# Optimization experiments

Hardware: AMD Instinct MI355X
Metric: run time of the kernel (lower is better)

Reference implementation:

```python
import jax, jax.numpy as jnp
import numpy as np

B = 4          # per_gpu_batch_size
P = 16         # n_contexts
N = B * P      # fused passage dim = 64
L = 512        # seq_len
H = 768        # hidden_size
S = 16         # sentence spans per passage


def setup_inputs() -> dict:
    key = jax.random.key(0)
    k1, k2, k3 = jax.random.split(key, 3)
    hidden_states = jax.random.normal(k1, (N, L, H), jnp.float32)
    # nn.Linear weight [out, in]; original init std=1.0 saturates tanh, use 0.02 scale for sane numerics
    dense_w = jax.random.normal(k2, (H, H), jnp.float32) * 0.02
    dense_b = jnp.zeros((H,), jnp.float32)
    attention_mask = jnp.ones((N, L), jnp.int32)
    # strictly increasing boundaries -> S non-empty, ragged, contiguous spans per passage
    r = jnp.sort(jax.random.randint(k3, (N, S + 1), 0, L - S), axis=-1) + jnp.arange(S + 1, dtype=jnp.int32)
    spans = jnp.stack([r[:, :-1], r[:, 1:]], axis=-1).astype(jnp.int32)  # [N, S, 2]
    return dict(hidden_states=hidden_states, dense_w=dense_w, dense_b=dense_b,
                attention_mask=attention_mask, spans=spans)


def reference(hidden_states, dense_w, dense_b, attention_mask, spans):
    # sentence_spans branch: token_tensor = hidden_states (all tokens)
    # pooled_output = activation(dense(token_tensor)); cls_norm_type == 'none' -> no norm
    pooled = jnp.tanh(jnp.einsum('nlh,oh->nlo', hidden_states, dense_w) + dense_b)  # [N, L, H]
    pooled_output_passages = pooled[:, 0]  # [N, H]
    # ragged per-span mean pooling, vectorized as a masked segment reduce
    pos = jnp.arange(L, dtype=jnp.int32)                         # [L]
    start = spans[..., 0][..., None]                             # [N, S, 1]
    end = spans[..., 1][..., None]                               # [N, S, 1]
    m = ((pos >= start) & (pos < end)).astype(pooled.dtype)      # [N, S, L]
    sums = jnp.einsum('nsl,nlh->nsh', m, pooled)                 # [N, S, H]
    counts = (spans[..., 1] - spans[..., 0]).astype(pooled.dtype)[..., None]  # [N, S, 1]
    sentence_embeddings = (sums / counts).reshape(N * S, H)      # [N*S, H]
    # all S spans valid per passage -> mask of zeros (0 = valid in original code)
    sentence_mask = jnp.zeros((N, S), jnp.float32)
    return pooled_output_passages, sentence_embeddings, sentence_mask
```

## Files before the change

### kernel.cpp

```cpp
#include <hip/hip_runtime.h>
#include <hip/hip_bf16.h>

#define NPASS 64
#define LSEQ  512
#define HDIM  768
#define NSPAN 16
#define MTOT  (NPASS*LSEQ)
#define OFF_SENT (NPASS*HDIM)
#define A_ELEMS (MTOT*HDIM)
#define W_ELEMS (HDIM*HDIM)

#define BM 128
#define BN 128
#define BK 32
#define NK (HDIM/BK)

typedef __bf16 bf16x8 __attribute__((ext_vector_type(8)));
typedef float  f32x4  __attribute__((ext_vector_type(4)));

__device__ inline unsigned short f2bf(float f) {
  __hip_bfloat16 h = __float2bfloat16(f);
  unsigned short u; __builtin_memcpy(&u, &h, 2); return u;
}

__device__ inline float fast_tanh(float x) {
  const float ax = fabsf(x);
  const float t  = __expf(-2.0f * ax);
  const float r  = (1.0f - t) * __builtin_amdgcn_rcpf(1.0f + t);
  return copysignf(r, x);
}

__global__ __launch_bounds__(256) void convert_kernel(
    const float* __restrict__ A, const float* __restrict__ W,
    unsigned short* __restrict__ Ab, unsigned short* __restrict__ Wb)
{
  const long long i = ((long long)blockIdx.x * 256 + threadIdx.x) * 8;
  const float* src; unsigned short* dst; long long off;
  if (i < A_ELEMS) { src = A; dst = Ab; off = i; }
  else             { src = W; dst = Wb; off = i - A_ELEMS; }
  const float4 a = *(const float4*)(src + off);
  const float4 b = *(const float4*)(src + off + 4);
  union { unsigned short us[8]; uint4 v; } o;
  o.us[0]=f2bf(a.x); o.us[1]=f2bf(a.y); o.us[2]=f2bf(a.z); o.us[3]=f2bf(a.w);
  o.us[4]=f2bf(b.x); o.us[5]=f2bf(b.y); o.us[6]=f2bf(b.z); o.us[7]=f2bf(b.w);
  *(uint4*)(dst + off) = o.v;
}

__global__ __launch_bounds__(256) void gemm_fused_kernel(
    const unsigned short* __restrict__ Ab,
    const unsigned short* __restrict__ Wb,
    const float* __restrict__ bias,
    const int* __restrict__ spans,
    float* __restrict__ out)
{
  __shared__ __align__(16) unsigned short As[2][BM*BK];
  __shared__ __align__(16) unsigned short Bs[2][BN*BK];
  __shared__ int   sp_st[NSPAN], sp_en[NSPAN];
  __shared__ float inv_s[NSPAN];
  __shared__ short sid_l[BM];
  __shared__ float bias_s[BN];

  const int tid  = threadIdx.x;
  const int wave = tid >> 6;
  const int lane = tid & 63;
  const int quad = lane >> 4;
  const int lr   = lane & 15;
  const int wm   = wave >> 1;
  const int wn   = wave & 1;
  const int tile_m = blockIdx.x * BM;
  const int tile_n = blockIdx.y * BN;
  const int npass  = tile_m >> 9;
  const int l0     = tile_m & 511;

  const int lrow = lane >> 2;
  const int lcol = (lane & 3) * 8;

  auto stage = [&](int k, int buf) {
    const int k0 = k * BK;
    #pragma unroll
    for (int j = 0; j < 4; ++j) {
      const int seg = wave * 4 + j;
      if (seg < 8) {
        const unsigned short* g =
            Ab + (size_t)(tile_m + seg * 16 + lrow) * HDIM + (k0 + lcol);
        __builtin_amdgcn_global_load_lds(
            (const __attribute__((address_space(1))) void*)g,
            (__attribute__((address_space(3))) void*)(As[buf] + seg * 512),
            16, 0, 0);
      } else {
        const int s2 = seg - 8;
        const unsigned short* g =
            Wb + (size_t)(tile_n + s2 * 16 + lrow) * HDIM + (k0 + lcol);
        __builtin_amdgcn_global_load_lds(
            (const __attribute__((address_space(1))) void*)g,
            (__attribute__((address_space(3))) void*)(Bs[buf] + s2 * 512),
            16, 0, 0);
      }
    }
  };

  stage(0, 0);
  if (tid < NSPAN) {
    const int st = spans[(npass * NSPAN + tid) * 2 + 0];
    const int en = spans[(npass * NSPAN + tid) * 2 + 1];
    sp_st[tid] = st; sp_en[tid] = en; inv_s[tid] = 1.0f / (float)(en - st);
  }
  if (tid >= 128 && tid < 128 + BN) bias_s[tid - 128] = bias[tile_n + tid - 128];
  __syncthreads();
  if (tid < BM) {
    const int l = l0 + tid;
    short s = -1;
    #pragma unroll
    for (int i = 0; i < NSPAN; ++i)
      if (l >= sp_st[i] && l < sp_en[i]) s = (short)i;
    sid_l[tid] = s;
  }

  f32x4 acc[4][4];
  #pragma unroll
  for (int i = 0; i < 4; ++i)
    #pragma unroll
    for (int j = 0; j < 4; ++j)
      acc[i][j] = (f32x4){0.f, 0.f, 0.f, 0.f};

  for (int k = 0; k < NK; ++k) {
    const int cur = k & 1;
    if (k + 1 < NK) stage(k + 1, cur ^ 1);

    bf16x8 af[4], bf[4];
    #pragma unroll
    for (int mt = 0; mt < 4; ++mt)
      af[mt] = *(const bf16x8*)(As[cur] + ((wm * 64 + mt * 16 + lr) * BK + quad * 8));
    #pragma unroll
    for (int nt = 0; nt < 4; ++nt)
      bf[nt] = *(const bf16x8*)(Bs[cur] + ((wn * 64 + nt * 16 + lr) * BK + quad * 8));

    #pragma unroll
    for (int mt = 0; mt < 4; ++mt)
      #pragma unroll
      for (int nt = 0; nt < 4; ++nt)
        acc[mt][nt] = __builtin_amdgcn_mfma_f32_16x16x32_bf16(
            af[mt], bf[nt], acc[mt][nt], 0, 0, 0);

    __syncthreads();
  }

  #pragma unroll
  for (int nt = 0; nt < 4; ++nt) {
    const int lcolo = wn * 64 + nt * 16 + lr;
    const int col   = tile_n + lcolo;
    const float bv  = bias_s[lcolo];
    float* sent_col = out + OFF_SENT + (size_t)(npass * NSPAN) * HDIM + col;
    #pragma unroll
    for (int mt = 0; mt < 4; ++mt) {
      const int rowbase = wm * 64 + mt * 16 + quad * 4;
      int prev = -1; float run = 0.f;
      #pragma unroll
      for (int r = 0; r < 4; ++r) {
        const int lrw = rowbase + r;
        const float v = fast_tanh(acc[mt][nt][r] + bv);
        if (l0 == 0 && lrw == 0) out[(size_t)npass * HDIM + col] = v;
        const int s = sid_l[lrw];
        if (s != prev) {
          if (prev >= 0) unsafeAtomicAdd(sent_col + (size_t)prev * HDIM, run * inv_s[prev]);
          prev = s; run = 0.f;
        }
        run += v;
      }
      if (prev >= 0) unsafeAtomicAdd(sent_col + (size_t)prev * HDIM, run * inv_s[prev]);
    }
  }
}

extern "C" void kernel_launch(void* const* d_in, const int* in_sizes, int n_in,
                              void* d_out, int out_size, void* d_ws, size_t ws_size,
                              hipStream_t stream) {
  const float* hs  = (const float*)d_in[0];
  const float* w   = (const float*)d_in[1];
  const float* bsc = (const float*)d_in[2];
  const int* spans = (const int*)d_in[4];
  float* out = (float*)d_out;

  unsigned short* Ab = (unsigned short*)d_ws;
  unsigned short* Wb = Ab + A_ELEMS;

  hipMemsetAsync(d_out, 0, (size_t)out_size * sizeof(float), stream);

  convert_kernel<<<dim3((A_ELEMS + W_ELEMS) / 8 / 256), dim3(256), 0, stream>>>(
      hs, w, Ab, Wb);

  dim3 grid(MTOT / BM, HDIM / BN);
  gemm_fused_kernel<<<grid, dim3(256), 0, stream>>>(Ab, Wb, bsc, spans, out);
}
```

Measured before the change: 268.0 us.

## Fuse fp32-to-bf16 activation conversion into GEMM staging with swizzled LDS

Removes the standalone pass that converted the full activation tensor to bf16. The GEMM now stages fp32 activations directly into LDS and converts them to bf16 in registers before the MFMA. XOR swizzles are added to the A and B LDS layouts to reduce bank conflicts. This saves a full read/write pass over the activations, but doubles the A bytes read per N-tile and doubles the LDS footprint for A, which may reduce occupancy.

```diff
diff --git a/kernel.cpp b/kernel.cpp
--- a/kernel.cpp
+++ b/kernel.cpp
@@ -7,7 +7,6 @@
 #define NSPAN 16
 #define MTOT  (NPASS*LSEQ)
 #define OFF_SENT (NPASS*HDIM)
-#define A_ELEMS (MTOT*HDIM)
 #define W_ELEMS (HDIM*HDIM)
 
 #define BM 128
@@ -16,6 +15,7 @@
 #define NK (HDIM/BK)
 
 typedef __bf16 bf16x8 __attribute__((ext_vector_type(8)));
+typedef __bf16 bf16x4 __attribute__((ext_vector_type(4)));
 typedef float  f32x4  __attribute__((ext_vector_type(4)));
 
 __device__ inline unsigned short f2bf(float f) {
@@ -30,30 +30,33 @@
   return copysignf(r, x);
 }
 
-__global__ __launch_bounds__(256) void convert_kernel(
-    const float* __restrict__ A, const float* __restrict__ W,
-    unsigned short* __restrict__ Ab, unsigned short* __restrict__ Wb)
+__device__ inline bf16x8 cvt8(f32x4 lo, f32x4 hi) {
+  union { bf16x4 h[2]; bf16x8 v; } u;
+  u.h[0] = __builtin_convertvector(lo, bf16x4);
+  u.h[1] = __builtin_convertvector(hi, bf16x4);
+  return u.v;
+}
+
+__global__ __launch_bounds__(256) void convert_w_kernel(
+    const float* __restrict__ W, unsigned short* __restrict__ Wb)
 {
-  const long long i = ((long long)blockIdx.x * 256 + threadIdx.x) * 8;
-  const float* src; unsigned short* dst; long long off;
-  if (i < A_ELEMS) { src = A; dst = Ab; off = i; }
-  else             { src = W; dst = Wb; off = i - A_ELEMS; }
-  const float4 a = *(const float4*)(src + off);
-  const float4 b = *(const float4*)(src + off + 4);
+  const int i = (blockIdx.x * 256 + threadIdx.x) * 8;
+  const float4 a = *(const float4*)(W + i);
+  const float4 b = *(const float4*)(W + i + 4);
   union { unsigned short us[8]; uint4 v; } o;
   o.us[0]=f2bf(a.x); o.us[1]=f2bf(a.y); o.us[2]=f2bf(a.z); o.us[3]=f2bf(a.w);
   o.us[4]=f2bf(b.x); o.us[5]=f2bf(b.y); o.us[6]=f2bf(b.z); o.us[7]=f2bf(b.w);
-  *(uint4*)(dst + off) = o.v;
+  *(uint4*)(Wb + i) = o.v;
 }
 
 __global__ __launch_bounds__(256) void gemm_fused_kernel(
-    const unsigned short* __restrict__ Ab,
+    const float* __restrict__ A,
     const unsigned short* __restrict__ Wb,
     const float* __restrict__ bias,
     const int* __restrict__ spans,
     float* __restrict__ out)
 {
-  __shared__ __align__(16) unsigned short As[2][BM*BK];
+  __shared__ __align__(16) float          As[2][BM*BK];
   __shared__ __align__(16) unsigned short Bs[2][BN*BK];
   __shared__ int   sp_st[NSPAN], sp_en[NSPAN];
   __shared__ float inv_s[NSPAN];
@@ -72,25 +75,25 @@
   const int npass  = tile_m >> 9;
   const int l0     = tile_m & 511;
 
-  const int lrow = lane >> 2;
-  const int lcol = (lane & 3) * 8;
-
   auto stage = [&](int k, int buf) {
     const int k0 = k * BK;
     #pragma unroll
-    for (int j = 0; j < 4; ++j) {
-      const int seg = wave * 4 + j;
-      if (seg < 8) {
-        const unsigned short* g =
-            Ab + (size_t)(tile_m + seg * 16 + lrow) * HDIM + (k0 + lcol);
+    for (int j = 0; j < 6; ++j) {
+      const int seg = j * 4 + wave;
+      if (seg < 16) {
+        const int row = seg * 8 + (lane >> 3);
+        const int gs  = (lane & 7) ^ ((lane >> 3) & 7);
+        const float* g = A + (size_t)(tile_m + row) * HDIM + (k0 + gs * 4);
         __builtin_amdgcn_global_load_lds(
             (const __attribute__((address_space(1))) void*)g,
-            (__attribute__((address_space(3))) void*)(As[buf] + seg * 512),
+            (__attribute__((address_space(3))) void*)(As[buf] + seg * 256),
             16, 0, 0);
       } else {
-        const int s2 = seg - 8;
+        const int s2  = seg - 16;
+        const int row = s2 * 16 + (lane >> 2);
+        const int gs  = (lane & 3) ^ ((lane >> 3) & 3);
         const unsigned short* g =
-            Wb + (size_t)(tile_n + s2 * 16 + lrow) * HDIM + (k0 + lcol);
+            Wb + (size_t)(tile_n + row) * HDIM + (k0 + gs * 8);
         __builtin_amdgcn_global_load_lds(
             (const __attribute__((address_space(1))) void*)g,
             (__attribute__((address_space(3))) void*)(Bs[buf] + s2 * 512),
@@ -127,20 +130,29 @@
     const int cur = k & 1;
     if (k + 1 < NK) stage(k + 1, cur ^ 1);
 
-    bf16x8 af[4], bf[4];
-    #pragma unroll
-    for (int mt = 0; mt < 4; ++mt)
-      af[mt] = *(const bf16x8*)(As[cur] + ((wm * 64 + mt * 16 + lr) * BK + quad * 8));
-    #pragma unroll
-    for (int nt = 0; nt < 4; ++nt)
-      bf[nt] = *(const bf16x8*)(Bs[cur] + ((wn * 64 + nt * 16 + lr) * BK + quad * 8));
+    bf16x8 af[4], bfr[4];
+    #pragma unroll
+    for (int mt = 0; mt < 4; ++mt) {
+      const int r  = wm * 64 + mt * 16 + lr;
+      const int sw = r & 7;
+      const float* base = As[cur] + r * BK;
+      const f32x4 lo = *(const f32x4*)(base + (((quad * 2    ) ^ sw) * 4));
+      const f32x4 hi = *(const f32x4*)(base + (((quad * 2 + 1) ^ sw) * 4));
+      af[mt] = cvt8(lo, hi);
+    }
+    #pragma unroll
+    for (int nt = 0; nt < 4; ++nt) {
+      const int r = wn * 64 + nt * 16 + lr;
+      const int g = quad ^ ((r >> 1) & 3);
+      bfr[nt] = *(const bf16x8*)(Bs[cur] + (r * BK + g * 8));
+    }
 
     #pragma unroll
     for (int mt = 0; mt < 4; ++mt)
       #pragma unroll
       for (int nt = 0; nt < 4; ++nt)
         acc[mt][nt] = __builtin_amdgcn_mfma_f32_16x16x32_bf16(
-            af[mt], bf[nt], acc[mt][nt], 0, 0, 0);
+            af[mt], bfr[nt], acc[mt][nt], 0, 0, 0);
 
     __syncthreads();
   }
@@ -181,14 +193,12 @@
   const int* spans = (const int*)d_in[4];
   float* out = (float*)d_out;
 
-  unsigned short* Ab = (unsigned short*)d_ws;
-  unsigned short* Wb = Ab + A_ELEMS;
+  unsigned short* Wb = (unsigned short*)d_ws;
 
   hipMemsetAsync(d_out, 0, (size_t)out_size * sizeof(float), stream);
 
-  convert_kernel<<<dim3((A_ELEMS + W_ELEMS) / 8 / 256), dim3(256), 0, stream>>>(
-      hs, w, Ab, Wb);
+  convert_w_kernel<<<dim3(W_ELEMS / 8 / 256), dim3(256), 0, stream>>>(w, Wb);
 
   dim3 grid(MTOT / BM, HDIM / BN);
-  gemm_fused_kernel<<<grid, dim3(256), 0, stream>>>(Ab, Wb, bsc, spans, out);
-}
+  gemm_fused_kernel<<<grid, dim3(256), 0, stream>>>(hs, Wb, bsc, spans, out);
+}
```

Result: no change. 269.7 us (+0.6%).

## Enlarge GEMM tiles to 256x256x64 with swizzled LDS and phased pipelining

Applied to the files above, without the earlier changes.

Rebuilds the fused GEMM around 256x256 output tiles with BK=64 and 512 threads (8 waves, each owning 128x64). Global-to-LDS loads use an XOR swizzle to avoid bank conflicts, and next-tile loads are interleaved across four compute phases with raw barriers and s_setprio around the MFMA bursts. A remapped 1D grid groups M blocks for L2 locality. The aim is more reuse per byte loaded and fewer sync stalls, at the cost of higher register and LDS pressure and fewer blocks (384) to spread across the CUs.

```diff
diff --git a/kernel.cpp b/kernel.cpp
--- a/kernel.cpp
+++ b/kernel.cpp
@@ -10,10 +10,12 @@
 #define A_ELEMS (MTOT*HDIM)
 #define W_ELEMS (HDIM*HDIM)
 
-#define BM 128
-#define BN 128
-#define BK 32
-#define NK (HDIM/BK)
+#define BM 256
+#define BN 256
+#define BK 64
+#define NKT (HDIM/BK)
+#define THREADS 512
+#define NBLK ((MTOT/BM)*(HDIM/BN))
 
 typedef __bf16 bf16x8 __attribute__((ext_vector_type(8)));
 typedef float  f32x4  __attribute__((ext_vector_type(4)));
@@ -46,18 +48,17 @@
   *(uint4*)(dst + off) = o.v;
 }
 
-__global__ __launch_bounds__(256) void gemm_fused_kernel(
+__global__ __launch_bounds__(THREADS, 2) void gemm_fused_kernel(
     const unsigned short* __restrict__ Ab,
     const unsigned short* __restrict__ Wb,
     const float* __restrict__ bias,
     const int* __restrict__ spans,
     float* __restrict__ out)
 {
-  __shared__ __align__(16) unsigned short As[2][BM*BK];
-  __shared__ __align__(16) unsigned short Bs[2][BN*BK];
-  __shared__ int   sp_st[NSPAN], sp_en[NSPAN];
+  __shared__ __align__(16) unsigned short As[2][2][128 * 64];
+  __shared__ __align__(16) unsigned short Bs[2][2][128 * 64];
+  __shared__ short sid_l[BM];
   __shared__ float inv_s[NSPAN];
-  __shared__ short sid_l[BM];
   __shared__ float bias_s[BN];
 
   const int tid  = threadIdx.x;
@@ -65,105 +66,135 @@
   const int lane = tid & 63;
   const int quad = lane >> 4;
   const int lr   = lane & 15;
-  const int wm   = wave >> 1;
-  const int wn   = wave & 1;
-  const int tile_m = blockIdx.x * BM;
-  const int tile_n = blockIdx.y * BN;
-  const int npass  = tile_m >> 9;
+  const int wm   = wave >> 2;
+  const int wn   = wave & 3;
+
+  const int b    = blockIdx.x;
+  const int mblk = (b & 7) * 16 + ((b >> 3) & 15);
+  const int nblk = b >> 7;
+  const int tile_m = mblk * BM;
+  const int tile_n = nblk * BN;
+  const int p      = tile_m >> 9;
   const int l0     = tile_m & 511;
 
-  const int lrow = lane >> 2;
-  const int lcol = (lane & 3) * 8;
-
-  auto stage = [&](int k, int buf) {
-    const int k0 = k * BK;
-    #pragma unroll
-    for (int j = 0; j < 4; ++j) {
-      const int seg = wave * 4 + j;
-      if (seg < 8) {
-        const unsigned short* g =
-            Ab + (size_t)(tile_m + seg * 16 + lrow) * HDIM + (k0 + lcol);
-        __builtin_amdgcn_global_load_lds(
-            (const __attribute__((address_space(1))) void*)g,
-            (__attribute__((address_space(3))) void*)(As[buf] + seg * 512),
-            16, 0, 0);
-      } else {
-        const int s2 = seg - 8;
-        const unsigned short* g =
-            Wb + (size_t)(tile_n + s2 * 16 + lrow) * HDIM + (k0 + lcol);
-        __builtin_amdgcn_global_load_lds(
-            (const __attribute__((address_space(1))) void*)g,
-            (__attribute__((address_space(3))) void*)(Bs[buf] + s2 * 512),
-            16, 0, 0);
-      }
+  auto stage_half = [&](const unsigned short* __restrict__ base_g, int row0g,
+                        int j, int h, unsigned short* lds_half) {
+    #pragma unroll
+    for (int l = 0; l < 2; ++l) {
+      const int gi = l * 512 + tid;
+      const int r  = gi >> 3;
+      const int g  = gi & 7;
+      const unsigned short* src =
+          base_g + (size_t)(row0g + h * 128 + r) * HDIM + j * BK + ((g ^ (r & 7)) * 8);
+      __builtin_amdgcn_global_load_lds(
+          (const __attribute__((address_space(1))) void*)src,
+          (__attribute__((address_space(3))) void*)(lds_half + gi * 8),
+          16, 0, 0);
     }
   };
 
-  stage(0, 0);
-  if (tid < NSPAN) {
-    const int st = spans[(npass * NSPAN + tid) * 2 + 0];
-    const int en = spans[(npass * NSPAN + tid) * 2 + 1];
-    sp_st[tid] = st; sp_en[tid] = en; inv_s[tid] = 1.0f / (float)(en - st);
-  }
-  if (tid >= 128 && tid < 128 + BN) bias_s[tid - 128] = bias[tile_n + tid - 128];
-  __syncthreads();
+  stage_half(Ab, tile_m, 0, 0, As[0][0]);
+  stage_half(Ab, tile_m, 0, 1, As[0][1]);
+  stage_half(Wb, tile_n, 0, 0, Bs[0][0]);
+  stage_half(Wb, tile_n, 0, 1, Bs[0][1]);
   if (tid < BM) {
     const int l = l0 + tid;
     short s = -1;
     #pragma unroll
-    for (int i = 0; i < NSPAN; ++i)
-      if (l >= sp_st[i] && l < sp_en[i]) s = (short)i;
+    for (int i = 0; i < NSPAN; ++i) {
+      const int st = spans[(p * NSPAN + i) * 2 + 0];
+      const int en = spans[(p * NSPAN + i) * 2 + 1];
+      if (l >= st && l < en) s = (short)i;
+    }
     sid_l[tid] = s;
+  } else {
+    bias_s[tid - 256] = bias[tile_n + tid - 256];
   }
-
-  f32x4 acc[4][4];
+  if (tid < NSPAN)
+    inv_s[tid] = 1.0f / (float)(spans[(p * NSPAN + tid) * 2 + 1] -
+                                spans[(p * NSPAN + tid) * 2 + 0]);
+  __syncthreads();
+
+  f32x4 acc[8][4];
   #pragma unroll
-  for (int i = 0; i < 4; ++i)
-    #pragma unroll
-    for (int j = 0; j < 4; ++j)
-      acc[i][j] = (f32x4){0.f, 0.f, 0.f, 0.f};
-
-  for (int k = 0; k < NK; ++k) {
-    const int cur = k & 1;
-    if (k + 1 < NK) stage(k + 1, cur ^ 1);
-
-    bf16x8 af[4], bf[4];
-    #pragma unroll
-    for (int mt = 0; mt < 4; ++mt)
-      af[mt] = *(const bf16x8*)(As[cur] + ((wm * 64 + mt * 16 + lr) * BK + quad * 8));
-    #pragma unroll
-    for (int nt = 0; nt < 4; ++nt)
-      bf[nt] = *(const bf16x8*)(Bs[cur] + ((wn * 64 + nt * 16 + lr) * BK + quad * 8));
-
-    #pragma unroll
-    for (int mt = 0; mt < 4; ++mt)
-      #pragma unroll
-      for (int nt = 0; nt < 4; ++nt)
-        acc[mt][nt] = __builtin_amdgcn_mfma_f32_16x16x32_bf16(
-            af[mt], bf[nt], acc[mt][nt], 0, 0, 0);
-
-    __syncthreads();
+  for (int i = 0; i < 8; ++i)
+    #pragma unroll
+    for (int jj = 0; jj < 4; ++jj)
+      acc[i][jj] = (f32x4){0.f, 0.f, 0.f, 0.f};
+
+  for (int j = 0; j < NKT; ++j) {
+    const int s = j & 1;
+    const unsigned short* Ah = As[s][wm];
+    const unsigned short* Bh = Bs[s][wn >> 1];
+    const int rbB = (wn & 1) * 64;
+
+    #pragma unroll
+    for (int ph = 0; ph < 4; ++ph) {
+      const int qm = ph >> 1, qn = ph & 1;
+
+      bf16x8 af[4][2], bfr[2][2];
+      #pragma unroll
+      for (int mt = 0; mt < 4; ++mt) {
+        const int r = qm * 64 + mt * 16 + lr;
+        #pragma unroll
+        for (int kk = 0; kk < 2; ++kk)
+          af[mt][kk] = *(const bf16x8*)(Ah + (r * 8 + ((kk * 4 + quad) ^ (r & 7))) * 8);
+      }
+      #pragma unroll
+      for (int nt = 0; nt < 2; ++nt) {
+        const int r = rbB + qn * 32 + nt * 16 + lr;
+        #pragma unroll
+        for (int kk = 0; kk < 2; ++kk)
+          bfr[nt][kk] = *(const bf16x8*)(Bh + (r * 8 + ((kk * 4 + quad) ^ (r & 7))) * 8);
+      }
+
+      if (j + 1 < NKT) {
+        if (ph == 0) {
+          stage_half(Ab, tile_m, j + 1, 0, As[s ^ 1][0]);
+          stage_half(Ab, tile_m, j + 1, 1, As[s ^ 1][1]);
+        } else if (ph == 1) {
+          stage_half(Wb, tile_n, j + 1, 0, Bs[s ^ 1][0]);
+          stage_half(Wb, tile_n, j + 1, 1, Bs[s ^ 1][1]);
+        }
+      }
+
+      __builtin_amdgcn_s_barrier();
+
+      __builtin_amdgcn_s_setprio(1);
+      #pragma unroll
+      for (int mt = 0; mt < 4; ++mt)
+        #pragma unroll
+        for (int nt = 0; nt < 2; ++nt)
+          #pragma unroll
+          for (int kk = 0; kk < 2; ++kk)
+            acc[qm * 4 + mt][qn * 2 + nt] = __builtin_amdgcn_mfma_f32_16x16x32_bf16(
+                af[mt][kk], bfr[nt][kk], acc[qm * 4 + mt][qn * 2 + nt], 0, 0, 0);
+      __builtin_amdgcn_s_setprio(0);
+
+      if (ph == 3) asm volatile("s_waitcnt vmcnt(0)" ::: "memory");
+      __builtin_amdgcn_s_barrier();
+    }
   }
 
   #pragma unroll
-  for (int nt = 0; nt < 4; ++nt) {
-    const int lcolo = wn * 64 + nt * 16 + lr;
-    const int col   = tile_n + lcolo;
-    const float bv  = bias_s[lcolo];
-    float* sent_col = out + OFF_SENT + (size_t)(npass * NSPAN) * HDIM + col;
-    #pragma unroll
-    for (int mt = 0; mt < 4; ++mt) {
-      const int rowbase = wm * 64 + mt * 16 + quad * 4;
+  for (int ntg = 0; ntg < 4; ++ntg) {
+    const int lcol = wn * 64 + ntg * 16 + lr;
+    const int col  = tile_n + lcol;
+    const float bv = bias_s[lcol];
+    float* sent_col = out + OFF_SENT + (size_t)(p * NSPAN) * HDIM + col;
+    #pragma unroll
+    for (int mtg = 0; mtg < 8; ++mtg) {
+      const int rowbase = wm * 128 + mtg * 16 + quad * 4;
       int prev = -1; float run = 0.f;
       #pragma unroll
       for (int r = 0; r < 4; ++r) {
-        const int lrw = rowbase + r;
-        const float v = fast_tanh(acc[mt][nt][r] + bv);
-        if (l0 == 0 && lrw == 0) out[(size_t)npass * HDIM + col] = v;
-        const int s = sid_l[lrw];
-        if (s != prev) {
+        const int row = rowbase + r;
+        const float v = fast_tanh(acc[mtg][ntg][r] + bv);
+        if (l0 == 0 && row == 0) out[(size_t)p * HDIM + col] = v;
+        const int sd = sid_l[row];
+        if (sd != prev) {
           if (prev >= 0) unsafeAtomicAdd(sent_col + (size_t)prev * HDIM, run * inv_s[prev]);
-          prev = s; run = 0.f;
+          prev = sd; run = 0.f;
         }
         run += v;
       }
@@ -189,6 +220,6 @@
   convert_kernel<<<dim3((A_ELEMS + W_ELEMS) / 8 / 256), dim3(256), 0, stream>>>(
       hs, w, Ab, Wb);
 
-  dim3 grid(MTOT / BM, HDIM / BN);
-  gemm_fused_kernel<<<grid, dim3(256), 0, stream>>>(Ab, Wb, bsc, spans, out);
-}
+  gemm_fused_kernel<<<dim3(NBLK), dim3(THREADS), 0, stream>>>(
+      Ab, Wb, bsc, spans, out);
+}
```

After: 270.8 us. No clear change (+1.0%).
